# Performance work log

Hardware: AMD Instinct MI355X
Metric: run time of the kernel (lower is better)

Reference implementation:

```python
import jax, jax.numpy as jnp
import numpy as np

L = 8          # number of GNN layers / graph variants
B = 128        # graphs per batch
NL = 32        # ligand nodes per graph
NP = 256       # protein nodes per graph
N_LIG = B * NL     # 4096
N_PROT = B * NP    # 32768
E_PL_G = 1024      # protein->ligand edges per graph
E_LL_G = 256       # ligand->ligand edges per graph
E_PL = B * E_PL_G  # 131072
E_LL = B * E_LL_G  # 32768
F_IN = 128
H = 256
OUT = 2


def _block_edges(key, n_per_graph, e_per_graph):
    # random node indices, offset so edges stay within each graph of the batch
    idx = jax.random.randint(key, (L, B, e_per_graph), 0, n_per_graph)
    off = (jnp.arange(B) * n_per_graph)[None, :, None]
    return (idx + off).reshape(L, B * e_per_graph).astype(jnp.int32)


def setup_inputs() -> dict:
    key = jax.random.key(0)
    ks = jax.random.split(key, 12)
    feat_lig = jax.random.normal(ks[0], (L, N_LIG, F_IN), jnp.float32)
    feat_prot = jax.random.normal(ks[1], (L, N_PROT, F_IN), jnp.float32)
    src_pl = _block_edges(ks[2], NP, E_PL_G)   # protein src indices
    dst_pl = _block_edges(ks[3], NL, E_PL_G)   # ligand dst indices
    src_ll = _block_edges(ks[4], NL, E_LL_G)
    dst_ll = _block_edges(ks[5], NL, E_LL_G)
    s = 1.0 / np.sqrt(F_IN)
    W_pl = jax.random.normal(ks[6], (L, F_IN, H), jnp.float32) * s
    b_pl = jnp.zeros((L, H), jnp.float32)
    W_ll = jax.random.normal(ks[7], (L, F_IN, H), jnp.float32) * s
    b_ll = jnp.zeros((L, H), jnp.float32)
    W_fc = jax.random.normal(ks[8], (L * H, OUT), jnp.float32) / np.sqrt(L * H)
    b_fc = jnp.zeros((OUT,), jnp.float32)
    return dict(feat_lig=feat_lig, feat_prot=feat_prot,
                src_pl=src_pl, dst_pl=dst_pl, src_ll=src_ll, dst_ll=dst_ll,
                W_pl=W_pl, b_pl=b_pl, W_ll=W_ll, b_ll=b_ll,
                W_fc=W_fc, b_fc=b_fc)


def _gconv(x_src, W, b, src, dst, n_src, n_dst):
    # DGL GraphConv with norm='both': D_dst^-1/2 * A^T * D_src^-1/2 * X W + b
    ones = jnp.ones(src.shape[0], x_src.dtype)
    deg_src = jnp.clip(jax.ops.segment_sum(ones, src, num_segments=n_src), 1.0)
    deg_dst = jnp.clip(jax.ops.segment_sum(ones, dst, num_segments=n_dst), 1.0)
    xw = (x_src * jax.lax.rsqrt(deg_src)[:, None]) @ W          # [n_src,H]
    agg = jax.ops.segment_sum(xw[src], dst, num_segments=n_dst)  # [n_dst,H]
    return agg * jax.lax.rsqrt(deg_dst)[:, None] + b


def reference(feat_lig, feat_prot, src_pl, dst_pl, src_ll, dst_ll,
              W_pl, b_pl, W_ll, b_ll, W_fc, b_fc):
    def layer(fl, fp, Wp, bp, Wl, bl, spl, dpl, sll, dll):
        # HeteroGraphConv sum-aggregates the two relations with dst='ligand'
        h = (_gconv(fp, Wp, bp, spl, dpl, N_PROT, N_LIG)
             + _gconv(fl, Wl, bl, sll, dll, N_LIG, N_LIG))      # [N_LIG,H]
        # unbatch + per-graph mean over ligand nodes (equal-size graphs)
        return h.reshape(B, NL, H).mean(axis=1)                  # [B,H]

    h8 = jax.vmap(layer)(feat_lig, feat_prot, W_pl, b_pl, W_ll, b_ll,
                         src_pl, dst_pl, src_ll, dst_ll)         # [L,B,H]
    combined = jnp.transpose(h8, (1, 0, 2)).reshape(B, L * H)    # cat dim=1
    return jax.nn.sigmoid(combined @ W_fc + b_fc)                # [B,OUT]
```

## Files before the change

### kernel.cpp

```cpp
#include <hip/hip_runtime.h>

#define L 8
#define B 128
#define NL 32
#define NP 256
#define EPL_G 1024
#define ELL_G 256
#define FIN 128
#define H 256
#define OUT 2

template <int REL>
__global__ __launch_bounds__(512) void gather_kernel(
    const float* __restrict__ feat,
    const int* __restrict__ srcA,
    const int* __restrict__ dstA,
    float* __restrict__ gout)
{
    constexpr int E  = (REL == 0) ? EPL_G : ELL_G;
    constexpr int NS = (REL == 0) ? NP : NL;

    const int l   = blockIdx.x >> 7;
    const int b   = blockIdx.x & 127;
    const int tid = threadIdx.x;

    __shared__ int   s_src[E];
    __shared__ int   s_dst[E];
    __shared__ float s_w[E];
    __shared__ int   s_cnt_src[NS];
    __shared__ int   s_cnt_dst[NL];
    __shared__ float s_red[8 * FIN];

    const int* srcp = srcA + (size_t)l * (B * E) + (size_t)b * E;
    const int* dstp = dstA + (size_t)l * (B * E) + (size_t)b * E;
    const float* fbase = feat + (size_t)l * (B * NS) * FIN;

    for (int i = tid; i < NS; i += 512) s_cnt_src[i] = 0;
    for (int i = tid; i < NL; i += 512) s_cnt_dst[i] = 0;
    __syncthreads();

    for (int e = tid; e < E; e += 512) {
        int s = srcp[e] - b * NS;
        int d = dstp[e] - b * NL;
        s_src[e] = s;
        s_dst[e] = d;
        atomicAdd(&s_cnt_src[s], 1);
        atomicAdd(&s_cnt_dst[d], 1);
    }
    __syncthreads();

    for (int e = tid; e < E; e += 512) {
        s_w[e] = rsqrtf((float)s_cnt_src[s_src[e]]) *
                 rsqrtf((float)s_cnt_dst[s_dst[e]]);
    }
    __syncthreads();

    const int lane = tid & 63;
    const int slot = tid >> 6;
    float acc0 = 0.f, acc1 = 0.f;
#pragma unroll 4
    for (int e = slot; e < E; e += 8) {
        int   s = s_src[e];
        float w = s_w[e];
        float2 v = *(const float2*)(
            fbase + (size_t)(b * NS + s) * FIN + lane * 2);
        acc0 += w * v.x;
        acc1 += w * v.y;
    }
    s_red[slot * FIN + lane * 2]     = acc0;
    s_red[slot * FIN + lane * 2 + 1] = acc1;
    __syncthreads();

    if (tid < FIN) {
        float t = 0.f;
#pragma unroll
        for (int k = 0; k < 8; k++) t += s_red[k * FIN + tid];
        gout[((size_t)l * B + b) * FIN + tid] = t * (1.0f / NL);
    }
}

__global__ __launch_bounds__(256) void wcomb_kernel(
    const float* __restrict__ W_pl,
    const float* __restrict__ W_ll,
    const float* __restrict__ W_fc,
    float* __restrict__ Wc_pl, float* __restrict__ Wc_ll)
{
    const int l = blockIdx.x;
    const float* W = blockIdx.y ? W_ll : W_pl;
    float* outc    = blockIdx.y ? Wc_ll : Wc_pl;
    const int t = threadIdx.x;
    const int f = t >> 1, o = t & 1;
    const float* wrow = W + ((size_t)l * FIN + f) * H;
    const float* fc   = W_fc + (size_t)l * H * OUT + o;
    float acc = 0.f;
#pragma unroll 4
    for (int h = 0; h < H; h++)
        acc += wrow[h] * fc[h * OUT];
    outc[((size_t)l * FIN + f) * OUT + o] = acc;
}

__global__ __launch_bounds__(256) void bias_kernel(
    const float* __restrict__ b_pl,
    const float* __restrict__ b_ll,
    const float* __restrict__ W_fc,
    const float* __restrict__ b_fc,
    float* __restrict__ bias_out)
{
    const int t = threadIdx.x;
    float a0 = 0.f, a1 = 0.f;
    for (int i = t; i < L * H; i += 256) {
        float bs = b_pl[i] + b_ll[i];
        a0 += bs * W_fc[i * OUT];
        a1 += bs * W_fc[i * OUT + 1];
    }
    __shared__ float r0[256], r1[256];
    r0[t] = a0; r1[t] = a1;
    __syncthreads();
    for (int s = 128; s > 0; s >>= 1) {
        if (t < s) { r0[t] += r0[t + s]; r1[t] += r1[t + s]; }
        __syncthreads();
    }
    if (t == 0) {
        bias_out[0] = r0[0] + b_fc[0];
        bias_out[1] = r1[0] + b_fc[1];
    }
}

__global__ __launch_bounds__(256) void final_kernel(
    const float* __restrict__ g_pl, const float* __restrict__ g_ll,
    const float* __restrict__ Wc_pl, const float* __restrict__ Wc_ll,
    const float* __restrict__ bias_out, float* __restrict__ out)
{
    const int b = blockIdx.x;
    const int t = threadIdx.x;
    const int o = t >> 7, f = t & 127;
    float acc = 0.f;
#pragma unroll
    for (int l = 0; l < L; l++) {
        float gp = g_pl[((size_t)l * B + b) * FIN + f];
        float gl = g_ll[((size_t)l * B + b) * FIN + f];
        acc += gp * Wc_pl[((size_t)l * FIN + f) * OUT + o]
             + gl * Wc_ll[((size_t)l * FIN + f) * OUT + o];
    }
    __shared__ float red[256];
    red[t] = acc;
    __syncthreads();
    for (int s = 64; s > 0; s >>= 1) {
        if (f < s) red[t] += red[t + s];
        __syncthreads();
    }
    if (f == 0) {
        float x = red[o << 7] + bias_out[o];
        out[b * OUT + o] = 1.0f / (1.0f + expf(-x));
    }
}

extern "C" void kernel_launch(void* const* d_in, const int* in_sizes, int n_in,
                              void* d_out, int out_size, void* d_ws, size_t ws_size,
                              hipStream_t stream) {
    const float* feat_lig  = (const float*)d_in[0];
    const float* feat_prot = (const float*)d_in[1];
    const int* src_pl = (const int*)d_in[2];
    const int* dst_pl = (const int*)d_in[3];
    const int* src_ll = (const int*)d_in[4];
    const int* dst_ll = (const int*)d_in[5];
    const float* W_pl = (const float*)d_in[6];
    const float* b_pl = (const float*)d_in[7];
    const float* W_ll = (const float*)d_in[8];
    const float* b_ll = (const float*)d_in[9];
    const float* W_fc = (const float*)d_in[10];
    const float* b_fc = (const float*)d_in[11];
    float* out = (float*)d_out;

    float* ws       = (float*)d_ws;
    float* g_pl     = ws;
    float* g_ll     = g_pl + (size_t)L * B * FIN;
    float* Wc_pl    = g_ll + (size_t)L * B * FIN;
    float* Wc_ll    = Wc_pl + (size_t)L * FIN * OUT;
    float* bias_out = Wc_ll + (size_t)L * FIN * OUT;

    gather_kernel<0><<<dim3(L * B), 512, 0, stream>>>(feat_prot, src_pl, dst_pl, g_pl);
    gather_kernel<1><<<dim3(L * B), 512, 0, stream>>>(feat_lig, src_ll, dst_ll, g_ll);
    wcomb_kernel<<<dim3(L, 2), 256, 0, stream>>>(W_pl, W_ll, W_fc, Wc_pl, Wc_ll);
    bias_kernel<<<1, 256, 0, stream>>>(b_pl, b_ll, W_fc, b_fc, bias_out);
    final_kernel<<<B, 256, 0, stream>>>(g_pl, g_ll, Wc_pl, Wc_ll, bias_out, out);
}
```

Measured before the change: 279.4 us.

## Precompute per-source-node coefficients and stream features densely in one fused launch

Each source node's combined edge weight (sum of dst-degree normalisations times src-degree normalisation and the mean factor) is now accumulated once in shared memory. Features are then read as a dense contiguous scan over all source nodes with float4 loads, instead of one gather per edge. The two gather relations plus the weight-combine and bias kernels are merged into a single launch using block-index ranges, leaving two launches total. This replaces 1024 random row reads per protein graph with 256 sequential ones, at the cost of extra shared-memory atomics.

```diff
diff --git a/kernel.cpp b/kernel.cpp
--- a/kernel.cpp
+++ b/kernel.cpp
@@ -10,119 +10,125 @@
 #define H 256
 #define OUT 2
 
-template <int REL>
-__global__ __launch_bounds__(512) void gather_kernel(
-    const float* __restrict__ feat,
-    const int* __restrict__ srcA,
-    const int* __restrict__ dstA,
-    float* __restrict__ gout)
+__global__ __launch_bounds__(512) void mega_kernel(
+    const float* __restrict__ feat_lig, const float* __restrict__ feat_prot,
+    const int* __restrict__ src_pl, const int* __restrict__ dst_pl,
+    const int* __restrict__ src_ll, const int* __restrict__ dst_ll,
+    const float* __restrict__ W_pl, const float* __restrict__ W_ll,
+    const float* __restrict__ W_fc,
+    const float* __restrict__ b_pl, const float* __restrict__ b_ll,
+    const float* __restrict__ b_fc,
+    float* __restrict__ g_pl, float* __restrict__ g_ll,
+    float* __restrict__ Wc_pl, float* __restrict__ Wc_ll,
+    float* __restrict__ bias_out)
 {
-    constexpr int E  = (REL == 0) ? EPL_G : ELL_G;
-    constexpr int NS = (REL == 0) ? NP : NL;
+    __shared__ int    s_cnt_src[NP];
+    __shared__ int    s_cnt_dst[NL];
+    __shared__ float  s_c[NP];
+    __shared__ float4 s_red[16][32];
 
-    const int l   = blockIdx.x >> 7;
-    const int b   = blockIdx.x & 127;
+    const int bid = blockIdx.x;
     const int tid = threadIdx.x;
 
-    __shared__ int   s_src[E];
-    __shared__ int   s_dst[E];
-    __shared__ float s_w[E];
-    __shared__ int   s_cnt_src[NS];
-    __shared__ int   s_cnt_dst[NL];
-    __shared__ float s_red[8 * FIN];
+    if (bid < 2 * L * B) {
+        const int rel = bid >> 10;
+        const int lb  = bid & 1023;
+        const int l = lb >> 7, b = lb & 127;
+        const int E  = rel ? ELL_G : EPL_G;
+        const int NS = rel ? NL : NP;
+        const float* feat = rel ? feat_lig : feat_prot;
+        const int* srcA   = rel ? src_ll : src_pl;
+        const int* dstA   = rel ? dst_ll : dst_pl;
+        float* gout       = rel ? g_ll : g_pl;
 
-    const int* srcp = srcA + (size_t)l * (B * E) + (size_t)b * E;
-    const int* dstp = dstA + (size_t)l * (B * E) + (size_t)b * E;
-    const float* fbase = feat + (size_t)l * (B * NS) * FIN;
+        const int* srcp = srcA + (size_t)l * (B * E) + (size_t)b * E;
+        const int* dstp = dstA + (size_t)l * (B * E) + (size_t)b * E;
 
-    for (int i = tid; i < NS; i += 512) s_cnt_src[i] = 0;
-    for (int i = tid; i < NL; i += 512) s_cnt_dst[i] = 0;
-    __syncthreads();
+        for (int i = tid; i < NS; i += 512) { s_cnt_src[i] = 0; s_c[i] = 0.f; }
+        if (tid < NL) s_cnt_dst[tid] = 0;
+        __syncthreads();
 
-    for (int e = tid; e < E; e += 512) {
-        int s = srcp[e] - b * NS;
-        int d = dstp[e] - b * NL;
-        s_src[e] = s;
-        s_dst[e] = d;
-        atomicAdd(&s_cnt_src[s], 1);
-        atomicAdd(&s_cnt_dst[d], 1);
-    }
-    __syncthreads();
+        int es[2], ed[2];
+        int ne = 0;
+        for (int e = tid; e < E; e += 512) {
+            int s = srcp[e] - b * NS;
+            int d = dstp[e] - b * NL;
+            es[ne] = s; ed[ne] = d; ne++;
+            atomicAdd(&s_cnt_src[s], 1);
+            atomicAdd(&s_cnt_dst[d], 1);
+        }
+        __syncthreads();
+        for (int i = 0; i < ne; i++)
+            atomicAdd(&s_c[es[i]], rsqrtf((float)s_cnt_dst[ed[i]]));
+        __syncthreads();
+        for (int i = tid; i < NS; i += 512) {
+            int c = s_cnt_src[i];
+            s_c[i] = c ? s_c[i] * rsqrtf((float)c) * (1.0f / NL) : 0.f;
+        }
+        __syncthreads();
 
-    for (int e = tid; e < E; e += 512) {
-        s_w[e] = rsqrtf((float)s_cnt_src[s_src[e]]) *
-                 rsqrtf((float)s_cnt_dst[s_dst[e]]);
-    }
-    __syncthreads();
+        const int lane = tid & 63;
+        const int wave = tid >> 6;
+        const int half = lane >> 5;
+        const int col  = lane & 31;
+        const int slot = wave * 2 + half;
+        const float* fb = feat + ((size_t)(l * B + b)) * NS * FIN;
 
-    const int lane = tid & 63;
-    const int slot = tid >> 6;
-    float acc0 = 0.f, acc1 = 0.f;
+        float4 acc = make_float4(0.f, 0.f, 0.f, 0.f);
 #pragma unroll 4
-    for (int e = slot; e < E; e += 8) {
-        int   s = s_src[e];
-        float w = s_w[e];
-        float2 v = *(const float2*)(
-            fbase + (size_t)(b * NS + s) * FIN + lane * 2);
-        acc0 += w * v.x;
-        acc1 += w * v.y;
-    }
-    s_red[slot * FIN + lane * 2]     = acc0;
-    s_red[slot * FIN + lane * 2 + 1] = acc1;
-    __syncthreads();
+        for (int r0 = 0; r0 < NS; r0 += 16) {
+            int r = r0 + slot;
+            float w = s_c[r];
+            float4 v = *(const float4*)(fb + (size_t)r * FIN + col * 4);
+            acc.x += w * v.x; acc.y += w * v.y;
+            acc.z += w * v.z; acc.w += w * v.w;
+        }
+        s_red[slot][col] = acc;
+        __syncthreads();
 
-    if (tid < FIN) {
-        float t = 0.f;
+        if (tid < FIN) {
+            float t = 0.f;
 #pragma unroll
-        for (int k = 0; k < 8; k++) t += s_red[k * FIN + tid];
-        gout[((size_t)l * B + b) * FIN + tid] = t * (1.0f / NL);
-    }
-}
-
-__global__ __launch_bounds__(256) void wcomb_kernel(
-    const float* __restrict__ W_pl,
-    const float* __restrict__ W_ll,
-    const float* __restrict__ W_fc,
-    float* __restrict__ Wc_pl, float* __restrict__ Wc_ll)
-{
-    const int l = blockIdx.x;
-    const float* W = blockIdx.y ? W_ll : W_pl;
-    float* outc    = blockIdx.y ? Wc_ll : Wc_pl;
-    const int t = threadIdx.x;
-    const int f = t >> 1, o = t & 1;
-    const float* wrow = W + ((size_t)l * FIN + f) * H;
-    const float* fc   = W_fc + (size_t)l * H * OUT + o;
-    float acc = 0.f;
+            for (int k = 0; k < 16; k++) {
+                const float* p = (const float*)&s_red[k][tid >> 2];
+                t += p[tid & 3];
+            }
+            gout[((size_t)(l * B + b)) * FIN + tid] = t;
+        }
+    } else if (bid < 2 * L * B + 16) {
+        const int q = bid - 2 * L * B;
+        const int l = q & 7;
+        const float* W = (q >> 3) ? W_ll : W_pl;
+        float* outc    = (q >> 3) ? Wc_ll : Wc_pl;
+        if (tid < 256) {
+            const int f = tid >> 1, o = tid & 1;
+            const float* wrow = W + ((size_t)l * FIN + f) * H;
+            const float* fc   = W_fc + (size_t)l * H * OUT + o;
+            float acc = 0.f;
 #pragma unroll 4
-    for (int h = 0; h < H; h++)
-        acc += wrow[h] * fc[h * OUT];
-    outc[((size_t)l * FIN + f) * OUT + o] = acc;
-}
-
-__global__ __launch_bounds__(256) void bias_kernel(
-    const float* __restrict__ b_pl,
-    const float* __restrict__ b_ll,
-    const float* __restrict__ W_fc,
-    const float* __restrict__ b_fc,
-    float* __restrict__ bias_out)
-{
-    const int t = threadIdx.x;
-    float a0 = 0.f, a1 = 0.f;
-    for (int i = t; i < L * H; i += 256) {
-        float bs = b_pl[i] + b_ll[i];
-        a0 += bs * W_fc[i * OUT];
-        a1 += bs * W_fc[i * OUT + 1];
-    }
-    __shared__ float r0[256], r1[256];
-    r0[t] = a0; r1[t] = a1;
-    __syncthreads();
-    for (int s = 128; s > 0; s >>= 1) {
-        if (t < s) { r0[t] += r0[t + s]; r1[t] += r1[t + s]; }
+            for (int h = 0; h < H; h++)
+                acc += wrow[h] * fc[h * OUT];
+            outc[((size_t)l * FIN + f) * OUT + o] = acc;
+        }
+    } else {
+        float* r0 = (float*)s_red;
+        float* r1 = r0 + 512;
+        float a0 = 0.f, a1 = 0.f;
+        for (int i = tid; i < L * H; i += 512) {
+            float bs = b_pl[i] + b_ll[i];
+            a0 += bs * W_fc[i * OUT];
+            a1 += bs * W_fc[i * OUT + 1];
+        }
+        r0[tid] = a0; r1[tid] = a1;
         __syncthreads();
-    }
-    if (t == 0) {
-        bias_out[0] = r0[0] + b_fc[0];
-        bias_out[1] = r1[0] + b_fc[1];
+        for (int s = 256; s > 0; s >>= 1) {
+            if (tid < s) { r0[tid] += r0[tid + s]; r1[tid] += r1[tid + s]; }
+            __syncthreads();
+        }
+        if (tid == 0) {
+            bias_out[0] = r0[0] + b_fc[0];
+            bias_out[1] = r1[0] + b_fc[1];
+        }
     }
 }
 
@@ -137,8 +143,8 @@
     float acc = 0.f;
 #pragma unroll
     for (int l = 0; l < L; l++) {
-        float gp = g_pl[((size_t)l * B + b) * FIN + f];
-        float gl = g_ll[((size_t)l * B + b) * FIN + f];
+        float gp = g_pl[((size_t)(l * B + b)) * FIN + f];
+        float gl = g_ll[((size_t)(l * B + b)) * FIN + f];
         acc += gp * Wc_pl[((size_t)l * FIN + f) * OUT + o]
              + gl * Wc_ll[((size_t)l * FIN + f) * OUT + o];
     }
@@ -179,9 +185,9 @@
     float* Wc_ll    = Wc_pl + (size_t)L * FIN * OUT;
     float* bias_out = Wc_ll + (size_t)L * FIN * OUT;
 
-    gather_kernel<0><<<dim3(L * B), 512, 0, stream>>>(feat_prot, src_pl, dst_pl, g_pl);
-    gather_kernel<1><<<dim3(L * B), 512, 0, stream>>>(feat_lig, src_ll, dst_ll, g_ll);
-    wcomb_kernel<<<dim3(L, 2), 256, 0, stream>>>(W_pl, W_ll, W_fc, Wc_pl, Wc_ll);
-    bias_kernel<<<1, 256, 0, stream>>>(b_pl, b_ll, W_fc, b_fc, bias_out);
-    final_kernel<<<B, 256, 0, stream>>>(g_pl, g_ll, Wc_pl, Wc_ll, bias_out, out);
+    mega_kernel<<<dim3(2 * L * B + 17), 512, 0, stream>>>(
+        feat_lig, feat_prot, src_pl, dst_pl, src_ll, dst_ll,
+        W_pl, W_ll, W_fc, b_pl, b_ll, b_fc,
+        g_pl, g_ll, Wc_pl, Wc_ll, bias_out);
+    final_kernel<<<dim3(B), 256, 0, stream>>>(g_pl, g_ll, Wc_pl, Wc_ll, bias_out, out);
 }
```

Result: faster. 240.4 us (-13.9%).
